# Performance work log

Hardware: AMD Instinct MI355X
Metric: run time of the kernel (lower is better)

## Reference

```python
import jax, jax.numpy as jnp
import numpy as np

N_NODES = 65536
N_EDGES = 1048576
IN_CH, HID_CH, OUT_CH = 300, 64, 20
DROPOUT_P = 0.5


def setup_inputs() -> dict:
    key = jax.random.key(0)
    ks = jax.random.split(key, 6)
    x = jax.random.normal(ks[0], (N_NODES, IN_CH), dtype=jnp.float32)
    edge_index = jax.random.randint(ks[1], (2, N_EDGES), 0, N_NODES, dtype=jnp.int64)
    edge_weight = jax.random.uniform(ks[2], (N_EDGES,), dtype=jnp.float32)
    # Glorot-ish init for linear weights (PyG lin has no bias; GCNConv adds its own bias)
    W1 = jax.random.normal(ks[3], (IN_CH, HID_CH), dtype=jnp.float32) / np.sqrt(IN_CH)
    b1 = jnp.zeros((HID_CH,), dtype=jnp.float32)
    W2 = jax.random.normal(ks[4], (HID_CH, OUT_CH), dtype=jnp.float32) / np.sqrt(HID_CH)
    b2 = jnp.zeros((OUT_CH,), dtype=jnp.float32)
    return {"x": x, "edge_index": edge_index, "edge_weight": edge_weight,
            "W1": W1, "b1": b1, "W2": W2, "b2": b2}


def _gcn_conv(x, src, dst, edge_weight, W, b, num_nodes):
    # GCNConv with add_self_loops=False, normalize=False:
    #   h = x @ W; out[i] = sum_{e: dst(e)=i} w_e * h[src(e)]; out += b
    h = x @ W                                   # [N, C_out]
    msg = h[src] * edge_weight[:, None]         # [E, C_out]
    agg = jax.ops.segment_sum(msg, dst, num_segments=num_nodes)
    return agg + b


def reference(x, edge_index, edge_weight, W1, b1, W2, b2):
    num_nodes = x.shape[0]
    src, dst = edge_index[0], edge_index[1]
    h = _gcn_conv(x, src, dst, edge_weight, W1, b1, num_nodes)
    h = jax.nn.relu(h)
    # dropout p=0.5, training=True, deterministic fixed key
    keep = jax.random.bernoulli(jax.random.key(42), 1.0 - DROPOUT_P, h.shape)
    h = jnp.where(keep, h / (1.0 - DROPOUT_P), 0.0)
    out = _gcn_conv(h, src, dst, edge_weight, W2, b2, num_nodes)
    return out
```

## Files before the change

### kernel.cpp

```cpp
#include <hip/hip_runtime.h>

#define N_NODES 65536
#define N_EDGES 1048576
#define NB 256
#define CAP 4608
#define EPB_A 4096
#define BLK_A (N_EDGES / EPB_A)
#define EPT_A (EPB_A / 1024)
#define GEMM_BLK (N_NODES / 64)

typedef __attribute__((ext_vector_type(8))) short short8v;
typedef __attribute__((ext_vector_type(4))) float float4v;

__device__ __forceinline__ unsigned short f2bf(float f) {
  unsigned u = __float_as_uint(f);
  unsigned r = u + 0x7FFFu + ((u >> 16) & 1u);
  return (unsigned short)(r >> 16);
}
__device__ __forceinline__ float bflo(unsigned u) { return __uint_as_float(u << 16); }
__device__ __forceinline__ float bfhi(unsigned u) { return __uint_as_float(u & 0xFFFF0000u); }

__device__ __forceinline__ bool keep_mask(unsigned idx) {
  const unsigned k0 = 0u, k1 = 42u;
  const unsigned k2 = 0x1BD11BDAu ^ k0 ^ k1;
  unsigned x0 = 0u;
  unsigned x1 = idx;
  x0 += k0; x1 += k1;
#define TF_ROUND(r) { x0 += x1; x1 = (x1 << (r)) | (x1 >> (32 - (r))); x1 ^= x0; }
  TF_ROUND(13) TF_ROUND(15) TF_ROUND(26) TF_ROUND(6)
  x0 += k1; x1 += k2 + 1u;
  TF_ROUND(17) TF_ROUND(29) TF_ROUND(16) TF_ROUND(24)
  x0 += k2; x1 += k0 + 2u;
  TF_ROUND(13) TF_ROUND(15) TF_ROUND(26) TF_ROUND(6)
  x0 += k0; x1 += k1 + 3u;
  TF_ROUND(17) TF_ROUND(29) TF_ROUND(16) TF_ROUND(24)
  x0 += k1; x1 += k2 + 4u;
  TF_ROUND(13) TF_ROUND(15) TF_ROUND(26) TF_ROUND(6)
  x0 += k2; x1 += k0 + 5u;
#undef TF_ROUND
  return ((x0 ^ x1) & 0x80000000u) == 0u;
}

__global__ __launch_bounds__(256) void prep_w1(const float* __restrict__ W1,
                                               unsigned short* __restrict__ Wt,
                                               unsigned* __restrict__ gcur) {
  if (blockIdx.x == 0) gcur[threadIdx.x] = 0u;
  int i = blockIdx.x * 256 + threadIdx.x;
  if (i >= 64 * 320) return;
  int ch = i / 320, k = i % 320;
  float v = (k < 300) ? W1[k * 64 + ch] : 0.0f;
  Wt[i] = f2bf(v);
}

__global__ __launch_bounds__(1024) void bin_pass(const int* __restrict__ ei,
                                                 const float* __restrict__ ew,
                                                 unsigned* __restrict__ gcur,
                                                 uint2* __restrict__ binned) {
  __shared__ unsigned cnt[NB], lofs[NB], lcur[NB], gbase[NB];
  __shared__ uint2 stage[EPB_A];
  const int t = threadIdx.x;
  const int e0 = blockIdx.x * EPB_A;
  if (t < NB) { cnt[t] = 0u; lcur[t] = 0u; }
  __syncthreads();
  unsigned pk[EPT_A], pw[EPT_A];
#pragma unroll
  for (int j = 0; j < EPT_A; ++j) {
    int e = e0 + t + j * 1024;
    unsigned s = (unsigned)ei[e];
    unsigned d = (unsigned)ei[N_EDGES + e];
    pk[j] = s | (d << 16);
    pw[j] = __float_as_uint(ew[e]);
    atomicAdd(&cnt[d >> 8], 1u);
  }
  __syncthreads();
  if (t < NB) lofs[t] = cnt[t];
  __syncthreads();
  for (int d = 1; d < NB; d <<= 1) {
    unsigned u = 0u;
    if (t < NB && t >= d) u = lofs[t - d];
    __syncthreads();
    if (t < NB) lofs[t] += u;
    __syncthreads();
  }
  if (t < NB) {
    unsigned incl = lofs[t];
    lofs[t] = incl - cnt[t];
    gbase[t] = (unsigned)t * CAP + atomicAdd(&gcur[t], cnt[t]);
  }
  __syncthreads();
#pragma unroll
  for (int j = 0; j < EPT_A; ++j) {
    unsigned b = pk[j] >> 24;
    unsigned slot = lofs[b] + atomicAdd(&lcur[b], 1u);
    stage[slot] = make_uint2(pk[j], pw[j]);
  }
  __syncthreads();
  for (int s = t; s < EPB_A; s += 1024) {
    uint2 u = stage[s];
    unsigned b = u.x >> 24;
    binned[gbase[b] + ((unsigned)s - lofs[b])] = u;
  }
}

__global__ __launch_bounds__(1024) void bucket_sort(const unsigned* __restrict__ gcur,
                                                    const uint2* __restrict__ binned,
                                                    unsigned* __restrict__ sortedc,
                                                    unsigned* __restrict__ offs_p) {
  __shared__ uint2 eLDS[CAP];
  __shared__ unsigned cnt[NB], cur[NB];
  const int t = threadIdx.x;
  const int b = blockIdx.x;
  const unsigned lo = (unsigned)b * CAP;
  const unsigned n_edges = gcur[b];
  if (t < NB) cnt[t] = 0u;
  __syncthreads();
  for (unsigned i = t; i < n_edges; i += 1024) {
    uint2 u = binned[lo + i];
    eLDS[i] = u;
    atomicAdd(&cnt[(u.x >> 16) & 255u], 1u);
  }
  __syncthreads();
  if (t < NB) cur[t] = cnt[t];
  __syncthreads();
  for (int d = 1; d < NB; d <<= 1) {
    unsigned u = 0u;
    if (t < NB && t >= d) u = cur[t - d];
    __syncthreads();
    if (t < NB) cur[t] += u;
    __syncthreads();
  }
  unsigned excl = 0u;
  if (t < NB) {
    excl = cur[t] - cnt[t];
    offs_p[b * NB + t] = (lo + excl) | (cnt[t] << 21);
  }
  __syncthreads();
  if (t < NB) cur[t] = excl;
  __syncthreads();
  for (unsigned i = t; i < n_edges; i += 1024) {
    uint2 u = eLDS[i];
    unsigned lo8 = (u.x >> 16) & 255u;
    unsigned p = lo + atomicAdd(&cur[lo8], 1u);
    sortedc[p] = (u.x & 0xFFFFu) | ((unsigned)f2bf(__uint_as_float(u.y)) << 16);
  }
}

__global__ __launch_bounds__(256) void gemm1(const float* __restrict__ x,
                                             const unsigned short* __restrict__ Wt,
                                             unsigned short* __restrict__ h1b) {
  __shared__ unsigned short As[64][72];
  __shared__ unsigned short Bs[64][72];
  const int t = threadIdx.x;
  const int node0 = blockIdx.x * 64;
  const int wave = t >> 6, lane = t & 63;
  const int quad = lane >> 4, l16 = lane & 15;
  float4v acc[4] = {{0.f,0.f,0.f,0.f},{0.f,0.f,0.f,0.f},{0.f,0.f,0.f,0.f},{0.f,0.f,0.f,0.f}};

  for (int kt = 0; kt < 5; ++kt) {
    const int k0 = kt * 64;
    for (int f = t; f < 1024; f += 256) {
      int node = f >> 4;
      int k = (f & 15) * 4;
      uint2 packed;
      if (k0 + k < 300) {
        float4 v = *(const float4*)(x + (size_t)(node0 + node) * 300 + k0 + k);
        packed.x = (unsigned)f2bf(v.x) | ((unsigned)f2bf(v.y) << 16);
        packed.y = (unsigned)f2bf(v.z) | ((unsigned)f2bf(v.w) << 16);
      } else {
        packed.x = 0u; packed.y = 0u;
      }
      *(uint2*)&As[node][k] = packed;
    }
    for (int f = t; f < 512; f += 256) {
      int ch = f >> 3;
      int kq = f & 7;
      uint4 v = *(const uint4*)(Wt + (size_t)ch * 320 + k0 + kq * 8);
      *(uint4*)&Bs[ch][kq * 8] = v;
    }
    __syncthreads();
    short8v a0 = *(const short8v*)&As[wave * 16 + l16][quad * 8];
    short8v a1 = *(const short8v*)&As[wave * 16 + l16][32 + quad * 8];
#pragma unroll
    for (int nt = 0; nt < 4; ++nt) {
      short8v b0 = *(const short8v*)&Bs[nt * 16 + l16][quad * 8];
      short8v b1 = *(const short8v*)&Bs[nt * 16 + l16][32 + quad * 8];
      acc[nt] = __builtin_amdgcn_mfma_f32_16x16x32_bf16(a0, b0, acc[nt], 0, 0, 0);
      acc[nt] = __builtin_amdgcn_mfma_f32_16x16x32_bf16(a1, b1, acc[nt], 0, 0, 0);
    }
    __syncthreads();
  }
#pragma unroll
  for (int nt = 0; nt < 4; ++nt) {
#pragma unroll
    for (int r = 0; r < 4; ++r) {
      h1b[(size_t)(node0 + wave * 16 + quad * 4 + r) * 64 + nt * 16 + l16] = f2bf(acc[nt][r]);
    }
  }
}

__global__ __launch_bounds__(256) void agg1_gemm2(const unsigned* __restrict__ offs_p,
                                                  const unsigned* __restrict__ sortedc,
                                                  const unsigned short* __restrict__ h1b,
                                                  const float* __restrict__ b1,
                                                  const float* __restrict__ W2,
                                                  unsigned* __restrict__ g32u) {
  __shared__ float h2[16][68];
  __shared__ float w2t[20][68];
  const int t = threadIdx.x;
  const int node0 = blockIdx.x * 16;
  for (int i = t; i < 20 * 64; i += 256) {
    int row = i >> 6, col = i & 63;
    w2t[row][col] = W2[col * 20 + row];
  }
  const int n = t >> 4, cg = t & 15;
  const int node = node0 + n;
  const unsigned op = offs_p[node];
  const unsigned s = op & 0x1FFFFFu;
  const unsigned e_end = s + (op >> 21);
  float4 acc = *(const float4*)(b1 + cg * 4);
  unsigned i = s;
  for (; i + 8 <= e_end; i += 8) {
    unsigned e0 = sortedc[i],     e1 = sortedc[i + 1], e2 = sortedc[i + 2], e3 = sortedc[i + 3];
    unsigned e4 = sortedc[i + 4], e5 = sortedc[i + 5], e6 = sortedc[i + 6], e7 = sortedc[i + 7];
    uint2 v0 = *(const uint2*)(h1b + ((size_t)(e0 & 0xFFFFu)) * 64 + cg * 4);
    uint2 v1 = *(const uint2*)(h1b + ((size_t)(e1 & 0xFFFFu)) * 64 + cg * 4);
    uint2 v2 = *(const uint2*)(h1b + ((size_t)(e2 & 0xFFFFu)) * 64 + cg * 4);
    uint2 v3 = *(const uint2*)(h1b + ((size_t)(e3 & 0xFFFFu)) * 64 + cg * 4);
    uint2 v4 = *(const uint2*)(h1b + ((size_t)(e4 & 0xFFFFu)) * 64 + cg * 4);
    uint2 v5 = *(const uint2*)(h1b + ((size_t)(e5 & 0xFFFFu)) * 64 + cg * 4);
    uint2 v6 = *(const uint2*)(h1b + ((size_t)(e6 & 0xFFFFu)) * 64 + cg * 4);
    uint2 v7 = *(const uint2*)(h1b + ((size_t)(e7 & 0xFFFFu)) * 64 + cg * 4);
    float w0 = bfhi(e0), w1 = bfhi(e1), w2 = bfhi(e2), w3 = bfhi(e3);
    float w4 = bfhi(e4), w5 = bfhi(e5), w6 = bfhi(e6), w7 = bfhi(e7);
    acc.x = fmaf(w0, bflo(v0.x), acc.x); acc.y = fmaf(w0, bfhi(v0.x), acc.y);
    acc.z = fmaf(w0, bflo(v0.y), acc.z); acc.w = fmaf(w0, bfhi(v0.y), acc.w);
    acc.x = fmaf(w1, bflo(v1.x), acc.x); acc.y = fmaf(w1, bfhi(v1.x), acc.y);
    acc.z = fmaf(w1, bflo(v1.y), acc.z); acc.w = fmaf(w1, bfhi(v1.y), acc.w);
    acc.x = fmaf(w2, bflo(v2.x), acc.x); acc.y = fmaf(w2, bfhi(v2.x), acc.y);
    acc.z = fmaf(w2, bflo(v2.y), acc.z); acc.w = fmaf(w2, bfhi(v2.y), acc.w);
    acc.x = fmaf(w3, bflo(v3.x), acc.x); acc.y = fmaf(w3, bfhi(v3.x), acc.y);
    acc.z = fmaf(w3, bflo(v3.y), acc.z); acc.w = fmaf(w3, bfhi(v3.y), acc.w);
    acc.x = fmaf(w4, bflo(v4.x), acc.x); acc.y = fmaf(w4, bfhi(v4.x), acc.y);
    acc.z = fmaf(w4, bflo(v4.y), acc.z); acc.w = fmaf(w4, bfhi(v4.y), acc.w);
    acc.x = fmaf(w5, bflo(v5.x), acc.x); acc.y = fmaf(w5, bfhi(v5.x), acc.y);
    acc.z = fmaf(w5, bflo(v5.y), acc.z); acc.w = fmaf(w5, bfhi(v5.y), acc.w);
    acc.x = fmaf(w6, bflo(v6.x), acc.x); acc.y = fmaf(w6, bfhi(v6.x), acc.y);
    acc.z = fmaf(w6, bflo(v6.y), acc.z); acc.w = fmaf(w6, bfhi(v6.y), acc.w);
    acc.x = fmaf(w7, bflo(v7.x), acc.x); acc.y = fmaf(w7, bfhi(v7.x), acc.y);
    acc.z = fmaf(w7, bflo(v7.y), acc.z); acc.w = fmaf(w7, bfhi(v7.y), acc.w);
  }
  for (; i < e_end; ++i) {
    unsigned e0 = sortedc[i];
    uint2 v0 = *(const uint2*)(h1b + ((size_t)(e0 & 0xFFFFu)) * 64 + cg * 4);
    float w0 = bfhi(e0);
    acc.x = fmaf(w0, bflo(v0.x), acc.x); acc.y = fmaf(w0, bfhi(v0.x), acc.y);
    acc.z = fmaf(w0, bflo(v0.y), acc.z); acc.w = fmaf(w0, bfhi(v0.y), acc.w);
  }
  const unsigned gi = (unsigned)node * 64u + (unsigned)cg * 4u;
  float r[4] = {acc.x, acc.y, acc.z, acc.w};
#pragma unroll
  for (int j = 0; j < 4; ++j) {
    float v = fmaxf(r[j], 0.0f);
    h2[n][cg * 4 + j] = keep_mask(gi + j) ? v * 2.0f : 0.0f;
  }
  __syncthreads();
  float d0 = 0.0f, d1 = 0.0f;
  if (cg < 10) {
    const int c0 = cg * 2, c1 = cg * 2 + 1;
#pragma unroll
    for (int k = 0; k < 64; k += 4) {
      float4 hv = *(const float4*)(&h2[n][k]);
      float4 w0 = *(const float4*)(&w2t[c0][k]);
      float4 w1 = *(const float4*)(&w2t[c1][k]);
      d0 = fmaf(hv.x, w0.x, d0); d0 = fmaf(hv.y, w0.y, d0);
      d0 = fmaf(hv.z, w0.z, d0); d0 = fmaf(hv.w, w0.w, d0);
      d1 = fmaf(hv.x, w1.x, d1); d1 = fmaf(hv.y, w1.y, d1);
      d1 = fmaf(hv.z, w1.z, d1); d1 = fmaf(hv.w, w1.w, d1);
    }
  }
  unsigned packed = (cg < 10) ? ((unsigned)f2bf(d0) | ((unsigned)f2bf(d1) << 16)) : 0u;
  g32u[(size_t)node * 16 + cg] = packed;
}

__global__ __launch_bounds__(256) void aggregate2(const unsigned* __restrict__ offs_p,
                                                  const unsigned* __restrict__ sortedc,
                                                  const unsigned* __restrict__ g32u,
                                                  const float* __restrict__ b2,
                                                  float* __restrict__ out) {
  const int t = threadIdx.x;
  const int n = blockIdx.x * 16 + (t >> 4);
  const int cg = t & 15;
  const unsigned op = offs_p[n];
  const unsigned s = op & 0x1FFFFFu;
  const unsigned e_end = s + (op >> 21);
  float ax = 0.0f, ay = 0.0f;
  unsigned i = s;
  for (; i + 8 <= e_end; i += 8) {
    unsigned e0 = sortedc[i],     e1 = sortedc[i + 1], e2 = sortedc[i + 2], e3 = sortedc[i + 3];
    unsigned e4 = sortedc[i + 4], e5 = sortedc[i + 5], e6 = sortedc[i + 6], e7 = sortedc[i + 7];
    unsigned v0 = g32u[(size_t)(e0 & 0xFFFFu) * 16 + cg];
    unsigned v1 = g32u[(size_t)(e1 & 0xFFFFu) * 16 + cg];
    unsigned v2 = g32u[(size_t)(e2 & 0xFFFFu) * 16 + cg];
    unsigned v3 = g32u[(size_t)(e3 & 0xFFFFu) * 16 + cg];
    unsigned v4 = g32u[(size_t)(e4 & 0xFFFFu) * 16 + cg];
    unsigned v5 = g32u[(size_t)(e5 & 0xFFFFu) * 16 + cg];
    unsigned v6 = g32u[(size_t)(e6 & 0xFFFFu) * 16 + cg];
    unsigned v7 = g32u[(size_t)(e7 & 0xFFFFu) * 16 + cg];
    float w0 = bfhi(e0), w1 = bfhi(e1), w2 = bfhi(e2), w3 = bfhi(e3);
    float w4 = bfhi(e4), w5 = bfhi(e5), w6 = bfhi(e6), w7 = bfhi(e7);
    ax = fmaf(w0, bflo(v0), ax); ay = fmaf(w0, bfhi(v0), ay);
    ax = fmaf(w1, bflo(v1), ax); ay = fmaf(w1, bfhi(v1), ay);
    ax = fmaf(w2, bflo(v2), ax); ay = fmaf(w2, bfhi(v2), ay);
    ax = fmaf(w3, bflo(v3), ax); ay = fmaf(w3, bfhi(v3), ay);
    ax = fmaf(w4, bflo(v4), ax); ay = fmaf(w4, bfhi(v4), ay);
    ax = fmaf(w5, bflo(v5), ax); ay = fmaf(w5, bfhi(v5), ay);
    ax = fmaf(w6, bflo(v6), ax); ay = fmaf(w6, bfhi(v6), ay);
    ax = fmaf(w7, bflo(v7), ax); ay = fmaf(w7, bfhi(v7), ay);
  }
  for (; i < e_end; ++i) {
    unsigned e0 = sortedc[i];
    unsigned v0 = g32u[(size_t)(e0 & 0xFFFFu) * 16 + cg];
    float w0 = bfhi(e0);
    ax = fmaf(w0, bflo(v0), ax); ay = fmaf(w0, bfhi(v0), ay);
  }
  if (cg < 10) {
    float2 o = make_float2(ax + b2[cg * 2], ay + b2[cg * 2 + 1]);
    *(float2*)(out + (size_t)n * 20 + cg * 2) = o;
  }
}

extern "C" void kernel_launch(void* const* d_in, const int* in_sizes, int n_in,
                              void* d_out, int out_size, void* d_ws, size_t ws_size,
                              hipStream_t stream) {
  const float* x  = (const float*)d_in[0];
  const int*   ei = (const int*)d_in[1];
  const float* ew = (const float*)d_in[2];
  const float* W1 = (const float*)d_in[3];
  const float* b1 = (const float*)d_in[4];
  const float* W2 = (const float*)d_in[5];
  const float* b2 = (const float*)d_in[6];
  float* out = (float*)d_out;

  unsigned short* h1b     = (unsigned short*)d_ws;
  unsigned*       g32u    = (unsigned*)(h1b + (size_t)N_NODES * 64);
  uint2*          binned  = (uint2*)(g32u + (size_t)N_NODES * 16);
  unsigned*       sortedc = (unsigned*)(binned + (size_t)NB * CAP);
  unsigned*       offs_p  = sortedc + (size_t)NB * CAP;
  unsigned short* Wt      = (unsigned short*)(offs_p + N_NODES);
  unsigned*       gcur    = (unsigned*)(Wt + 64 * 320);

  prep_w1<<<(64 * 320 + 255) / 256, 256, 0, stream>>>(W1, Wt, gcur);
  bin_pass<<<BLK_A, 1024, 0, stream>>>(ei, ew, gcur, binned);
  bucket_sort<<<NB, 1024, 0, stream>>>(gcur, binned, sortedc, offs_p);
  gemm1<<<GEMM_BLK, 256, 0, stream>>>(x, Wt, h1b);
  agg1_gemm2<<<N_NODES / 16, 256, 0, stream>>>(offs_p, sortedc, h1b, b1, W2, g32u);
  aggregate2<<<N_NODES / 16, 256, 0, stream>>>(offs_p, sortedc, g32u, b2, out);
}
```

Baseline: 219.6 us.

## Replace bucket sort with per-bucket LDS atomic accumulation in both aggregations

Drops the bucket_sort kernel and the CSR offsets. Each of the 256 destination buckets is now handled by one 1024-thread block that accumulates edge messages into a shared-memory tile with float atomics. Layer 1 then applies bias, ReLU, dropout and the W2 projection from LDS, and layer 2 scatters similarly. This removes a kernel launch and the sorted-edge write/read, at the cost of LDS atomic contention, only 256 blocks of parallelism, and non-deterministic summation order.

Result: slower. 621.8 us (+183.1%).

```diff
diff --git a/kernel.cpp b/kernel.cpp
--- a/kernel.cpp
+++ b/kernel.cpp
@@ -8,6 +8,8 @@
 #define BLK_A (N_EDGES / EPB_A)
 #define EPT_A (EPB_A / 1024)
 #define GEMM_BLK (N_NODES / 64)
+#define A1_STRIDE 65
+#define A2_STRIDE 21
 
 typedef __attribute__((ext_vector_type(8))) short short8v;
 typedef __attribute__((ext_vector_type(4))) float float4v;
@@ -102,49 +104,6 @@
   }
 }
 
-__global__ __launch_bounds__(1024) void bucket_sort(const unsigned* __restrict__ gcur,
-                                                    const uint2* __restrict__ binned,
-                                                    unsigned* __restrict__ sortedc,
-                                                    unsigned* __restrict__ offs_p) {
-  __shared__ uint2 eLDS[CAP];
-  __shared__ unsigned cnt[NB], cur[NB];
-  const int t = threadIdx.x;
-  const int b = blockIdx.x;
-  const unsigned lo = (unsigned)b * CAP;
-  const unsigned n_edges = gcur[b];
-  if (t < NB) cnt[t] = 0u;
-  __syncthreads();
-  for (unsigned i = t; i < n_edges; i += 1024) {
-    uint2 u = binned[lo + i];
-    eLDS[i] = u;
-    atomicAdd(&cnt[(u.x >> 16) & 255u], 1u);
-  }
-  __syncthreads();
-  if (t < NB) cur[t] = cnt[t];
-  __syncthreads();
-  for (int d = 1; d < NB; d <<= 1) {
-    unsigned u = 0u;
-    if (t < NB && t >= d) u = cur[t - d];
-    __syncthreads();
-    if (t < NB) cur[t] += u;
-    __syncthreads();
-  }
-  unsigned excl = 0u;
-  if (t < NB) {
-    excl = cur[t] - cnt[t];
-    offs_p[b * NB + t] = (lo + excl) | (cnt[t] << 21);
-  }
-  __syncthreads();
-  if (t < NB) cur[t] = excl;
-  __syncthreads();
-  for (unsigned i = t; i < n_edges; i += 1024) {
-    uint2 u = eLDS[i];
-    unsigned lo8 = (u.x >> 16) & 255u;
-    unsigned p = lo + atomicAdd(&cur[lo8], 1u);
-    sortedc[p] = (u.x & 0xFFFFu) | ((unsigned)f2bf(__uint_as_float(u.y)) << 16);
-  }
-}
-
 __global__ __launch_bounds__(256) void gemm1(const float* __restrict__ x,
                                              const unsigned short* __restrict__ Wt,
                                              unsigned short* __restrict__ h1b) {
@@ -198,134 +157,94 @@
   }
 }
 
-__global__ __launch_bounds__(256) void agg1_gemm2(const unsigned* __restrict__ offs_p,
-                                                  const unsigned* __restrict__ sortedc,
-                                                  const unsigned short* __restrict__ h1b,
-                                                  const float* __restrict__ b1,
-                                                  const float* __restrict__ W2,
-                                                  unsigned* __restrict__ g32u) {
-  __shared__ float h2[16][68];
-  __shared__ float w2t[20][68];
-  const int t = threadIdx.x;
-  const int node0 = blockIdx.x * 16;
-  for (int i = t; i < 20 * 64; i += 256) {
-    int row = i >> 6, col = i & 63;
-    w2t[row][col] = W2[col * 20 + row];
-  }
-  const int n = t >> 4, cg = t & 15;
-  const int node = node0 + n;
-  const unsigned op = offs_p[node];
-  const unsigned s = op & 0x1FFFFFu;
-  const unsigned e_end = s + (op >> 21);
-  float4 acc = *(const float4*)(b1 + cg * 4);
-  unsigned i = s;
-  for (; i + 8 <= e_end; i += 8) {
-    unsigned e0 = sortedc[i],     e1 = sortedc[i + 1], e2 = sortedc[i + 2], e3 = sortedc[i + 3];
-    unsigned e4 = sortedc[i + 4], e5 = sortedc[i + 5], e6 = sortedc[i + 6], e7 = sortedc[i + 7];
-    uint2 v0 = *(const uint2*)(h1b + ((size_t)(e0 & 0xFFFFu)) * 64 + cg * 4);
-    uint2 v1 = *(const uint2*)(h1b + ((size_t)(e1 & 0xFFFFu)) * 64 + cg * 4);
-    uint2 v2 = *(const uint2*)(h1b + ((size_t)(e2 & 0xFFFFu)) * 64 + cg * 4);
-    uint2 v3 = *(const uint2*)(h1b + ((size_t)(e3 & 0xFFFFu)) * 64 + cg * 4);
-    uint2 v4 = *(const uint2*)(h1b + ((size_t)(e4 & 0xFFFFu)) * 64 + cg * 4);
-    uint2 v5 = *(const uint2*)(h1b + ((size_t)(e5 & 0xFFFFu)) * 64 + cg * 4);
-    uint2 v6 = *(const uint2*)(h1b + ((size_t)(e6 & 0xFFFFu)) * 64 + cg * 4);
-    uint2 v7 = *(const uint2*)(h1b + ((size_t)(e7 & 0xFFFFu)) * 64 + cg * 4);
-    float w0 = bfhi(e0), w1 = bfhi(e1), w2 = bfhi(e2), w3 = bfhi(e3);
-    float w4 = bfhi(e4), w5 = bfhi(e5), w6 = bfhi(e6), w7 = bfhi(e7);
-    acc.x = fmaf(w0, bflo(v0.x), acc.x); acc.y = fmaf(w0, bfhi(v0.x), acc.y);
-    acc.z = fmaf(w0, bflo(v0.y), acc.z); acc.w = fmaf(w0, bfhi(v0.y), acc.w);
-    acc.x = fmaf(w1, bflo(v1.x), acc.x); acc.y = fmaf(w1, bfhi(v1.x), acc.y);
-    acc.z = fmaf(w1, bflo(v1.y), acc.z); acc.w = fmaf(w1, bfhi(v1.y), acc.w);
-    acc.x = fmaf(w2, bflo(v2.x), acc.x); acc.y = fmaf(w2, bfhi(v2.x), acc.y);
-    acc.z = fmaf(w2, bflo(v2.y), acc.z); acc.w = fmaf(w2, bfhi(v2.y), acc.w);
-    acc.x = fmaf(w3, bflo(v3.x), acc.x); acc.y = fmaf(w3, bfhi(v3.x), acc.y);
-    acc.z = fmaf(w3, bflo(v3.y), acc.z); acc.w = fmaf(w3, bfhi(v3.y), acc.w);
-    acc.x = fmaf(w4, bflo(v4.x), acc.x); acc.y = fmaf(w4, bfhi(v4.x), acc.y);
-    acc.z = fmaf(w4, bflo(v4.y), acc.z); acc.w = fmaf(w4, bfhi(v4.y), acc.w);
-    acc.x = fmaf(w5, bflo(v5.x), acc.x); acc.y = fmaf(w5, bfhi(v5.x), acc.y);
-    acc.z = fmaf(w5, bflo(v5.y), acc.z); acc.w = fmaf(w5, bfhi(v5.y), acc.w);
-    acc.x = fmaf(w6, bflo(v6.x), acc.x); acc.y = fmaf(w6, bfhi(v6.x), acc.y);
-    acc.z = fmaf(w6, bflo(v6.y), acc.z); acc.w = fmaf(w6, bfhi(v6.y), acc.w);
-    acc.x = fmaf(w7, bflo(v7.x), acc.x); acc.y = fmaf(w7, bfhi(v7.x), acc.y);
-    acc.z = fmaf(w7, bflo(v7.y), acc.z); acc.w = fmaf(w7, bfhi(v7.y), acc.w);
-  }
-  for (; i < e_end; ++i) {
-    unsigned e0 = sortedc[i];
-    uint2 v0 = *(const uint2*)(h1b + ((size_t)(e0 & 0xFFFFu)) * 64 + cg * 4);
-    float w0 = bfhi(e0);
-    acc.x = fmaf(w0, bflo(v0.x), acc.x); acc.y = fmaf(w0, bfhi(v0.x), acc.y);
-    acc.z = fmaf(w0, bflo(v0.y), acc.z); acc.w = fmaf(w0, bfhi(v0.y), acc.w);
-  }
-  const unsigned gi = (unsigned)node * 64u + (unsigned)cg * 4u;
-  float r[4] = {acc.x, acc.y, acc.z, acc.w};
-#pragma unroll
-  for (int j = 0; j < 4; ++j) {
-    float v = fmaxf(r[j], 0.0f);
-    h2[n][cg * 4 + j] = keep_mask(gi + j) ? v * 2.0f : 0.0f;
-  }
-  __syncthreads();
-  float d0 = 0.0f, d1 = 0.0f;
-  if (cg < 10) {
-    const int c0 = cg * 2, c1 = cg * 2 + 1;
-#pragma unroll
-    for (int k = 0; k < 64; k += 4) {
-      float4 hv = *(const float4*)(&h2[n][k]);
-      float4 w0 = *(const float4*)(&w2t[c0][k]);
-      float4 w1 = *(const float4*)(&w2t[c1][k]);
-      d0 = fmaf(hv.x, w0.x, d0); d0 = fmaf(hv.y, w0.y, d0);
-      d0 = fmaf(hv.z, w0.z, d0); d0 = fmaf(hv.w, w0.w, d0);
-      d1 = fmaf(hv.x, w1.x, d1); d1 = fmaf(hv.y, w1.y, d1);
-      d1 = fmaf(hv.z, w1.z, d1); d1 = fmaf(hv.w, w1.w, d1);
-    }
-  }
-  unsigned packed = (cg < 10) ? ((unsigned)f2bf(d0) | ((unsigned)f2bf(d1) << 16)) : 0u;
-  g32u[(size_t)node * 16 + cg] = packed;
-}
-
-__global__ __launch_bounds__(256) void aggregate2(const unsigned* __restrict__ offs_p,
-                                                  const unsigned* __restrict__ sortedc,
-                                                  const unsigned* __restrict__ g32u,
-                                                  const float* __restrict__ b2,
-                                                  float* __restrict__ out) {
-  const int t = threadIdx.x;
-  const int n = blockIdx.x * 16 + (t >> 4);
-  const int cg = t & 15;
-  const unsigned op = offs_p[n];
-  const unsigned s = op & 0x1FFFFFu;
-  const unsigned e_end = s + (op >> 21);
-  float ax = 0.0f, ay = 0.0f;
-  unsigned i = s;
-  for (; i + 8 <= e_end; i += 8) {
-    unsigned e0 = sortedc[i],     e1 = sortedc[i + 1], e2 = sortedc[i + 2], e3 = sortedc[i + 3];
-    unsigned e4 = sortedc[i + 4], e5 = sortedc[i + 5], e6 = sortedc[i + 6], e7 = sortedc[i + 7];
-    unsigned v0 = g32u[(size_t)(e0 & 0xFFFFu) * 16 + cg];
-    unsigned v1 = g32u[(size_t)(e1 & 0xFFFFu) * 16 + cg];
-    unsigned v2 = g32u[(size_t)(e2 & 0xFFFFu) * 16 + cg];
-    unsigned v3 = g32u[(size_t)(e3 & 0xFFFFu) * 16 + cg];
-    unsigned v4 = g32u[(size_t)(e4 & 0xFFFFu) * 16 + cg];
-    unsigned v5 = g32u[(size_t)(e5 & 0xFFFFu) * 16 + cg];
-    unsigned v6 = g32u[(size_t)(e6 & 0xFFFFu) * 16 + cg];
-    unsigned v7 = g32u[(size_t)(e7 & 0xFFFFu) * 16 + cg];
-    float w0 = bfhi(e0), w1 = bfhi(e1), w2 = bfhi(e2), w3 = bfhi(e3);
-    float w4 = bfhi(e4), w5 = bfhi(e5), w6 = bfhi(e6), w7 = bfhi(e7);
-    ax = fmaf(w0, bflo(v0), ax); ay = fmaf(w0, bfhi(v0), ay);
-    ax = fmaf(w1, bflo(v1), ax); ay = fmaf(w1, bfhi(v1), ay);
-    ax = fmaf(w2, bflo(v2), ax); ay = fmaf(w2, bfhi(v2), ay);
-    ax = fmaf(w3, bflo(v3), ax); ay = fmaf(w3, bfhi(v3), ay);
-    ax = fmaf(w4, bflo(v4), ax); ay = fmaf(w4, bfhi(v4), ay);
-    ax = fmaf(w5, bflo(v5), ax); ay = fmaf(w5, bfhi(v5), ay);
-    ax = fmaf(w6, bflo(v6), ax); ay = fmaf(w6, bfhi(v6), ay);
-    ax = fmaf(w7, bflo(v7), ax); ay = fmaf(w7, bfhi(v7), ay);
-  }
-  for (; i < e_end; ++i) {
-    unsigned e0 = sortedc[i];
-    unsigned v0 = g32u[(size_t)(e0 & 0xFFFFu) * 16 + cg];
-    float w0 = bfhi(e0);
-    ax = fmaf(w0, bflo(v0), ax); ay = fmaf(w0, bfhi(v0), ay);
-  }
-  if (cg < 10) {
-    float2 o = make_float2(ax + b2[cg * 2], ay + b2[cg * 2 + 1]);
-    *(float2*)(out + (size_t)n * 20 + cg * 2) = o;
+__global__ __launch_bounds__(1024) void agg1_gemm2_b(const unsigned* __restrict__ gcur,
+                                                     const uint2* __restrict__ binned,
+                                                     const unsigned short* __restrict__ h1b,
+                                                     const float* __restrict__ b1,
+                                                     const float* __restrict__ W2,
+                                                     unsigned short* __restrict__ g16) {
+  __shared__ float acc[256 * A1_STRIDE];
+  __shared__ float w2t[20 * 68];
+  const int t = threadIdx.x;
+  const int b = blockIdx.x;
+  for (int i = t; i < 256 * A1_STRIDE; i += 1024) acc[i] = 0.0f;
+  for (int i = t; i < 20 * 64; i += 1024) {
+    int oc = i >> 6, k = i & 63;
+    w2t[oc * 68 + k] = W2[k * 20 + oc];
+  }
+  __syncthreads();
+  const unsigned lo = (unsigned)b * CAP;
+  const unsigned n_e = gcur[b];
+  const int eg = t >> 4, cg = t & 15;
+  for (unsigned i = eg; i < n_e; i += 64) {
+    uint2 u = binned[lo + i];
+    unsigned src = u.x & 0xFFFFu;
+    unsigned d8 = (u.x >> 16) & 0xFFu;
+    float w = __uint_as_float(u.y);
+    uint2 h = *(const uint2*)(h1b + ((size_t)src << 6) + cg * 4);
+    float* a = &acc[d8 * A1_STRIDE + cg * 4];
+    atomicAdd(&a[0], w * bflo(h.x));
+    atomicAdd(&a[1], w * bfhi(h.x));
+    atomicAdd(&a[2], w * bflo(h.y));
+    atomicAdd(&a[3], w * bfhi(h.y));
+  }
+  __syncthreads();
+  const int n = t >> 2, q = t & 3;
+  const unsigned node = (unsigned)b * 256u + (unsigned)n;
+#pragma unroll
+  for (int m = 0; m < 16; ++m) {
+    int ch = q * 16 + m;
+    float v = acc[n * A1_STRIDE + ch] + b1[ch];
+    v = fmaxf(v, 0.0f);
+    acc[n * A1_STRIDE + ch] = keep_mask(node * 64u + (unsigned)ch) ? v * 2.0f : 0.0f;
+  }
+  __syncthreads();
+  float s0 = 0.f, s1 = 0.f, s2 = 0.f, s3 = 0.f, s4 = 0.f;
+  for (int k = 0; k < 64; ++k) {
+    float h = acc[n * A1_STRIDE + k];
+    s0 = fmaf(h, w2t[(q     ) * 68 + k], s0);
+    s1 = fmaf(h, w2t[(q +  4) * 68 + k], s1);
+    s2 = fmaf(h, w2t[(q +  8) * 68 + k], s2);
+    s3 = fmaf(h, w2t[(q + 12) * 68 + k], s3);
+    s4 = fmaf(h, w2t[(q + 16) * 68 + k], s4);
+  }
+  unsigned short* gr = g16 + ((size_t)node << 5);
+  gr[q     ] = f2bf(s0);
+  gr[q +  4] = f2bf(s1);
+  gr[q +  8] = f2bf(s2);
+  gr[q + 12] = f2bf(s3);
+  gr[q + 16] = f2bf(s4);
+  gr[20 + q] = 0; gr[24 + q] = 0; gr[28 + q] = 0;
+}
+
+__global__ __launch_bounds__(1024) void agg2_b(const unsigned* __restrict__ gcur,
+                                               const uint2* __restrict__ binned,
+                                               const unsigned* __restrict__ g32u,
+                                               const float* __restrict__ b2,
+                                               float* __restrict__ out) {
+  __shared__ float acc2[256 * A2_STRIDE];
+  const int t = threadIdx.x;
+  const int b = blockIdx.x;
+  for (int i = t; i < 256 * A2_STRIDE; i += 1024) acc2[i] = 0.0f;
+  __syncthreads();
+  const unsigned lo = (unsigned)b * CAP;
+  const unsigned n_e = gcur[b];
+  const int eg = t >> 4, cg = t & 15;
+  for (unsigned i = eg; i < n_e; i += 64) {
+    uint2 u = binned[lo + i];
+    unsigned src = u.x & 0xFFFFu;
+    unsigned d8 = (u.x >> 16) & 0xFFu;
+    float w = __uint_as_float(u.y);
+    if (cg < 10) {
+      unsigned gv = g32u[((size_t)src << 4) + cg];
+      atomicAdd(&acc2[d8 * A2_STRIDE + cg * 2 + 0], w * bflo(gv));
+      atomicAdd(&acc2[d8 * A2_STRIDE + cg * 2 + 1], w * bfhi(gv));
+    }
+  }
+  __syncthreads();
+  for (int i = t; i < 256 * 20; i += 1024) {
+    int n = i / 20, ch = i % 20;
+    out[(size_t)((unsigned)b * 256u + (unsigned)n) * 20 + ch] = acc2[n * A2_STRIDE + ch] + b2[ch];
   }
 }
 
@@ -341,18 +260,15 @@
   const float* b2 = (const float*)d_in[6];
   float* out = (float*)d_out;
 
-  unsigned short* h1b     = (unsigned short*)d_ws;
-  unsigned*       g32u    = (unsigned*)(h1b + (size_t)N_NODES * 64);
-  uint2*          binned  = (uint2*)(g32u + (size_t)N_NODES * 16);
-  unsigned*       sortedc = (unsigned*)(binned + (size_t)NB * CAP);
-  unsigned*       offs_p  = sortedc + (size_t)NB * CAP;
-  unsigned short* Wt      = (unsigned short*)(offs_p + N_NODES);
-  unsigned*       gcur    = (unsigned*)(Wt + 64 * 320);
+  unsigned short* h1b    = (unsigned short*)d_ws;
+  unsigned short* g16    = h1b + (size_t)N_NODES * 64;
+  uint2*          binned = (uint2*)(g16 + (size_t)N_NODES * 32);
+  unsigned short* Wt     = (unsigned short*)(binned + (size_t)NB * CAP);
+  unsigned*       gcur   = (unsigned*)(Wt + 64 * 320);
 
   prep_w1<<<(64 * 320 + 255) / 256, 256, 0, stream>>>(W1, Wt, gcur);
   bin_pass<<<BLK_A, 1024, 0, stream>>>(ei, ew, gcur, binned);
-  bucket_sort<<<NB, 1024, 0, stream>>>(gcur, binned, sortedc, offs_p);
   gemm1<<<GEMM_BLK, 256, 0, stream>>>(x, Wt, h1b);
-  agg1_gemm2<<<N_NODES / 16, 256, 0, stream>>>(offs_p, sortedc, h1b, b1, W2, g32u);
-  aggregate2<<<N_NODES / 16, 256, 0, stream>>>(offs_p, sortedc, g32u, b2, out);
-}
+  agg1_gemm2_b<<<NB, 1024, 0, stream>>>(gcur, binned, h1b, b1, W2, g16);
+  agg2_b<<<NB, 1024, 0, stream>>>(gcur, binned, (const unsigned*)g16, b2, out);
+}
```

## Fuse weight prep into bin pass and co-launch bucket sort with GEMM1

Applied to the files above, without the earlier changes.

Drops the global atomic bucket cursor. Each bin block now writes its locally sorted tile plus per-bucket count and offset matrices, and bucket-sort blocks gather their slices using a prefix scan over those matrices. The W1 transpose is folded into extra blocks of the bin kernel, and bucket sort and GEMM1 share one launch through block-index dispatch with a union shared buffer. This cuts the launch count from six to four and lets the sort overlap the GEMM, at the cost of serial per-thread gather loops in the sort and only 256 threads for the sort work.

After: 216.2 us. No clear change (-1.5%).

```diff
diff --git a/kernel.cpp b/kernel.cpp
--- a/kernel.cpp
+++ b/kernel.cpp
@@ -7,6 +7,7 @@
 #define EPB_A 4096
 #define BLK_A (N_EDGES / EPB_A)
 #define EPT_A (EPB_A / 1024)
+#define WT_BLK 20
 #define GEMM_BLK (N_NODES / 64)
 
 typedef __attribute__((ext_vector_type(8))) short short8v;
@@ -41,25 +42,24 @@
   return ((x0 ^ x1) & 0x80000000u) == 0u;
 }
 
-__global__ __launch_bounds__(256) void prep_w1(const float* __restrict__ W1,
-                                               unsigned short* __restrict__ Wt,
-                                               unsigned* __restrict__ gcur) {
-  if (blockIdx.x == 0) gcur[threadIdx.x] = 0u;
-  int i = blockIdx.x * 256 + threadIdx.x;
-  if (i >= 64 * 320) return;
-  int ch = i / 320, k = i % 320;
-  float v = (k < 300) ? W1[k * 64 + ch] : 0.0f;
-  Wt[i] = f2bf(v);
-}
-
-__global__ __launch_bounds__(1024) void bin_pass(const int* __restrict__ ei,
+__global__ __launch_bounds__(1024) void binpass2(const int* __restrict__ ei,
                                                  const float* __restrict__ ew,
-                                                 unsigned* __restrict__ gcur,
-                                                 uint2* __restrict__ binned) {
-  __shared__ unsigned cnt[NB], lofs[NB], lcur[NB], gbase[NB];
+                                                 const float* __restrict__ W1,
+                                                 uint2* __restrict__ binned2,
+                                                 unsigned* __restrict__ cnt_mat,
+                                                 unsigned* __restrict__ lofs_mat,
+                                                 unsigned short* __restrict__ Wt) {
+  const int b = blockIdx.x;
+  const int t = threadIdx.x;
+  if (b >= BLK_A) {
+    int i = (b - BLK_A) * 1024 + t;
+    int ch = i / 320, k = i % 320;
+    Wt[i] = f2bf((k < 300) ? W1[k * 64 + ch] : 0.0f);
+    return;
+  }
+  __shared__ unsigned cnt[NB], lofs[NB], lcur[NB];
   __shared__ uint2 stage[EPB_A];
-  const int t = threadIdx.x;
-  const int e0 = blockIdx.x * EPB_A;
+  const int e0 = b * EPB_A;
   if (t < NB) { cnt[t] = 0u; lcur[t] = 0u; }
   __syncthreads();
   unsigned pk[EPT_A], pw[EPT_A];
@@ -83,61 +83,69 @@
     __syncthreads();
   }
   if (t < NB) {
-    unsigned incl = lofs[t];
-    lofs[t] = incl - cnt[t];
-    gbase[t] = (unsigned)t * CAP + atomicAdd(&gcur[t], cnt[t]);
+    lofs[t] -= cnt[t];
+    cnt_mat[(unsigned)b * NB + t]  = cnt[t];
+    lofs_mat[(unsigned)b * NB + t] = lofs[t];
   }
   __syncthreads();
 #pragma unroll
   for (int j = 0; j < EPT_A; ++j) {
-    unsigned b = pk[j] >> 24;
-    unsigned slot = lofs[b] + atomicAdd(&lcur[b], 1u);
+    unsigned bk = pk[j] >> 24;
+    unsigned slot = lofs[bk] + atomicAdd(&lcur[bk], 1u);
     stage[slot] = make_uint2(pk[j], pw[j]);
   }
   __syncthreads();
-  for (int s = t; s < EPB_A; s += 1024) {
-    uint2 u = stage[s];
-    unsigned b = u.x >> 24;
-    binned[gbase[b] + ((unsigned)s - lofs[b])] = u;
-  }
-}
-
-__global__ __launch_bounds__(1024) void bucket_sort(const unsigned* __restrict__ gcur,
-                                                    const uint2* __restrict__ binned,
-                                                    unsigned* __restrict__ sortedc,
-                                                    unsigned* __restrict__ offs_p) {
-  __shared__ uint2 eLDS[CAP];
-  __shared__ unsigned cnt[NB], cur[NB];
-  const int t = threadIdx.x;
-  const int b = blockIdx.x;
+  uint2* dst = binned2 + (size_t)b * EPB_A;
+  for (int s = t; s < EPB_A; s += 1024) dst[s] = stage[s];
+}
+
+__device__ __forceinline__ void bucket_body2(unsigned char* raw, int b,
+                                             const unsigned* __restrict__ cnt_mat,
+                                             const unsigned* __restrict__ lofs_mat,
+                                             const uint2* __restrict__ binned2,
+                                             unsigned* __restrict__ sortedc,
+                                             unsigned* __restrict__ offs_p) {
+  uint2*    eLDS = (uint2*)raw;
+  unsigned* cnt  = (unsigned*)(raw + 36864);
+  unsigned* cur  = cnt + NB;
+  unsigned* tot  = cur + NB;
+  const int t = threadIdx.x;
+  const unsigned scnt = cnt_mat[(unsigned)t * NB + b];
+  const unsigned sofs = lofs_mat[(unsigned)t * NB + b];
+  cnt[t] = 0u;
+  cur[t] = scnt;
+  __syncthreads();
+  for (int d = 1; d < NB; d <<= 1) {
+    unsigned u = (t >= d) ? cur[t - d] : 0u;
+    __syncthreads();
+    cur[t] += u;
+    __syncthreads();
+  }
+  const unsigned mystart = cur[t] - scnt;
+  if (t == NB - 1) *tot = cur[t];
+  __syncthreads();
+  const unsigned n_edges = *tot;
+  const uint2* src = binned2 + (size_t)t * EPB_A + sofs;
+  for (unsigned j = 0; j < scnt; ++j) eLDS[mystart + j] = src[j];
+  __syncthreads();
+  for (unsigned i = t; i < n_edges; i += 256)
+    atomicAdd(&cnt[(eLDS[i].x >> 16) & 255u], 1u);
+  __syncthreads();
+  cur[t] = cnt[t];
+  __syncthreads();
+  for (int d = 1; d < NB; d <<= 1) {
+    unsigned u = (t >= d) ? cur[t - d] : 0u;
+    __syncthreads();
+    cur[t] += u;
+    __syncthreads();
+  }
   const unsigned lo = (unsigned)b * CAP;
-  const unsigned n_edges = gcur[b];
-  if (t < NB) cnt[t] = 0u;
-  __syncthreads();
-  for (unsigned i = t; i < n_edges; i += 1024) {
-    uint2 u = binned[lo + i];
-    eLDS[i] = u;
-    atomicAdd(&cnt[(u.x >> 16) & 255u], 1u);
-  }
-  __syncthreads();
-  if (t < NB) cur[t] = cnt[t];
-  __syncthreads();
-  for (int d = 1; d < NB; d <<= 1) {
-    unsigned u = 0u;
-    if (t < NB && t >= d) u = cur[t - d];
-    __syncthreads();
-    if (t < NB) cur[t] += u;
-    __syncthreads();
-  }
-  unsigned excl = 0u;
-  if (t < NB) {
-    excl = cur[t] - cnt[t];
-    offs_p[b * NB + t] = (lo + excl) | (cnt[t] << 21);
-  }
-  __syncthreads();
-  if (t < NB) cur[t] = excl;
-  __syncthreads();
-  for (unsigned i = t; i < n_edges; i += 1024) {
+  unsigned excl = cur[t] - cnt[t];
+  offs_p[b * NB + t] = (lo + excl) | (cnt[t] << 21);
+  __syncthreads();
+  cur[t] = excl;
+  __syncthreads();
+  for (unsigned i = t; i < n_edges; i += 256) {
     uint2 u = eLDS[i];
     unsigned lo8 = (u.x >> 16) & 255u;
     unsigned p = lo + atomicAdd(&cur[lo8], 1u);
@@ -145,13 +153,14 @@
   }
 }
 
-__global__ __launch_bounds__(256) void gemm1(const float* __restrict__ x,
-                                             const unsigned short* __restrict__ Wt,
-                                             unsigned short* __restrict__ h1b) {
-  __shared__ unsigned short As[64][72];
-  __shared__ unsigned short Bs[64][72];
-  const int t = threadIdx.x;
-  const int node0 = blockIdx.x * 64;
+__device__ __forceinline__ void gemm1_body(unsigned char* smraw, int nb,
+                                           const float* __restrict__ x,
+                                           const unsigned short* __restrict__ Wt,
+                                           unsigned short* __restrict__ h1b) {
+  unsigned short (*As)[72] = (unsigned short (*)[72])smraw;
+  unsigned short (*Bs)[72] = (unsigned short (*)[72])(smraw + 9216);
+  const int t = threadIdx.x;
+  const int node0 = nb * 64;
   const int wave = t >> 6, lane = t & 63;
   const int quad = lane >> 4, l16 = lane & 15;
   float4v acc[4] = {{0.f,0.f,0.f,0.f},{0.f,0.f,0.f,0.f},{0.f,0.f,0.f,0.f},{0.f,0.f,0.f,0.f}};
@@ -195,6 +204,22 @@
     for (int r = 0; r < 4; ++r) {
       h1b[(size_t)(node0 + wave * 16 + quad * 4 + r) * 64 + nt * 16 + l16] = f2bf(acc[nt][r]);
     }
+  }
+}
+
+__global__ __launch_bounds__(256) void bucketsort_gemm1(const unsigned* __restrict__ cnt_mat,
+                                                        const unsigned* __restrict__ lofs_mat,
+                                                        const uint2* __restrict__ binned2,
+                                                        unsigned* __restrict__ sortedc,
+                                                        unsigned* __restrict__ offs_p,
+                                                        const float* __restrict__ x,
+                                                        const unsigned short* __restrict__ Wt,
+                                                        unsigned short* __restrict__ h1b) {
+  __shared__ __align__(16) unsigned char sm[38928];
+  if (blockIdx.x < NB) {
+    bucket_body2(sm, blockIdx.x, cnt_mat, lofs_mat, binned2, sortedc, offs_p);
+  } else {
+    gemm1_body(sm, blockIdx.x - NB, x, Wt, h1b);
   }
 }
 
@@ -341,18 +366,18 @@
   const float* b2 = (const float*)d_in[6];
   float* out = (float*)d_out;
 
-  unsigned short* h1b     = (unsigned short*)d_ws;
-  unsigned*       g32u    = (unsigned*)(h1b + (size_t)N_NODES * 64);
-  uint2*          binned  = (uint2*)(g32u + (size_t)N_NODES * 16);
-  unsigned*       sortedc = (unsigned*)(binned + (size_t)NB * CAP);
-  unsigned*       offs_p  = sortedc + (size_t)NB * CAP;
-  unsigned short* Wt      = (unsigned short*)(offs_p + N_NODES);
-  unsigned*       gcur    = (unsigned*)(Wt + 64 * 320);
-
-  prep_w1<<<(64 * 320 + 255) / 256, 256, 0, stream>>>(W1, Wt, gcur);
-  bin_pass<<<BLK_A, 1024, 0, stream>>>(ei, ew, gcur, binned);
-  bucket_sort<<<NB, 1024, 0, stream>>>(gcur, binned, sortedc, offs_p);
-  gemm1<<<GEMM_BLK, 256, 0, stream>>>(x, Wt, h1b);
+  unsigned short* h1b      = (unsigned short*)d_ws;
+  unsigned*       g32u     = (unsigned*)(h1b + (size_t)N_NODES * 64);
+  uint2*          binned2  = (uint2*)(g32u + (size_t)N_NODES * 16);
+  unsigned*       sortedc  = (unsigned*)(binned2 + (size_t)N_EDGES);
+  unsigned*       offs_p   = sortedc + (size_t)NB * CAP;
+  unsigned*       cnt_mat  = offs_p + N_NODES;
+  unsigned*       lofs_mat = cnt_mat + (size_t)BLK_A * NB;
+  unsigned short* Wt       = (unsigned short*)(lofs_mat + (size_t)BLK_A * NB);
+
+  binpass2<<<BLK_A + WT_BLK, 1024, 0, stream>>>(ei, ew, W1, binned2, cnt_mat, lofs_mat, Wt);
+  bucketsort_gemm1<<<NB + GEMM_BLK, 256, 0, stream>>>(cnt_mat, lofs_mat, binned2,
+                                                      sortedc, offs_p, x, Wt, h1b);
   agg1_gemm2<<<N_NODES / 16, 256, 0, stream>>>(offs_p, sortedc, h1b, b1, W2, g32u);
   aggregate2<<<N_NODES / 16, 256, 0, stream>>>(offs_p, sortedc, g32u, b2, out);
 }
```
